# Performance work log

Measured on AMD Instinct MI355X. Metric: run time of the kernel, lower is better.

The kernel has to match this reference:

```python
import jax, jax.numpy as jnp
import numpy as np

B, S, DIN, DOUT = 4, 2048, 4096, 4096

def setup_inputs() -> dict:
    key = jax.random.key(0)
    k1, k2, k3, k4 = jax.random.split(key, 4)
    x = jax.random.normal(k1, (B, S, DIN), dtype=jnp.float32)
    # int8-valued quantized weights in [-127, 127]
    weight_int8 = jax.random.randint(k2, (DOUT, DIN), -127, 128, dtype=jnp.int32).astype(jnp.int8)
    # per-output-row scales, positive, clamped at 1e-8 like the torch code
    weight_scale = jnp.maximum(jax.random.uniform(k3, (DOUT, 1), dtype=jnp.float32) * 0.01, 1e-8)
    bias = jax.random.normal(k4, (DOUT,), dtype=jnp.float32)
    return {"x": x, "weight_int8": weight_int8, "weight_scale": weight_scale, "bias": bias}

def reference(x, weight_int8, weight_scale, bias):
    # Dequantize: [DOUT, DIN] = int8 * per-row scale (broadcast over in_features)
    w = weight_int8.astype(x.dtype) * weight_scale.astype(x.dtype)
    # F.linear: y = x @ w.T + bias
    return jnp.einsum('bsd,od->bso', x, w) + bias
```

## Files before the change

### kernel.cpp

```cpp
#include <hip/hip_runtime.h>
#include <stdint.h>

#define MM 8192
#define NN 4096
#define KK 4096
#define BM 256
#define BN 256
#define BK 64
#define NT (KK / BK)
#define NHALF (4 * NT)

typedef short bf16x8 __attribute__((ext_vector_type(8)));
typedef float f32x4 __attribute__((ext_vector_type(4)));

__device__ __forceinline__ unsigned int f2bf(float f) {
    unsigned int u = __builtin_bit_cast(unsigned int, f);
    u += 0x7FFFu + ((u >> 16) & 1u);
    return u >> 16;
}

__global__ __launch_bounds__(256) void cvt_x_kernel(const float* __restrict__ x,
                                                    unsigned short* __restrict__ xb) {
    int i = blockIdx.x * blockDim.x + threadIdx.x;
    const float4* p = (const float4*)x + (size_t)i * 2;
    float4 a = p[0], b = p[1];
    uint4 o;
    o.x = f2bf(a.x) | (f2bf(a.y) << 16);
    o.y = f2bf(a.z) | (f2bf(a.w) << 16);
    o.z = f2bf(b.x) | (f2bf(b.y) << 16);
    o.w = f2bf(b.z) | (f2bf(b.w) << 16);
    ((uint4*)xb)[i] = o;
}

__global__ __launch_bounds__(256) void cvt_w_kernel(const int* __restrict__ w,
                                                    unsigned short* __restrict__ wb) {
    int i = blockIdx.x * blockDim.x + threadIdx.x;
    const int4* p = (const int4*)w + (size_t)i * 2;
    int4 a = p[0], b = p[1];
    uint4 o;
    o.x = f2bf((float)a.x) | (f2bf((float)a.y) << 16);
    o.y = f2bf((float)a.z) | (f2bf((float)a.w) << 16);
    o.z = f2bf((float)b.x) | (f2bf((float)b.y) << 16);
    o.w = f2bf((float)b.z) | (f2bf((float)b.w) << 16);
    ((uint4*)wb)[i] = o;
}

#define SWZ(q) ((q) ^ ((((q) >> 8) & 7) << 4))

__global__ __launch_bounds__(512, 2) void gemm_kernel(const unsigned short* __restrict__ A,
                                                      const unsigned short* __restrict__ Bt,
                                                      const float* __restrict__ scale,
                                                      const float* __restrict__ bias,
                                                      float* __restrict__ C) {
    __shared__ __align__(16) unsigned short As[2][BM * BK];
    __shared__ __align__(16) unsigned short Bs[2][BN * BK];

    const int nbn = NN / BN;
    const int cpx = ((MM / BM) * (NN / BN)) >> 3;
    int bid = blockIdx.x;
    int swzb = (bid & 7) * cpx + (bid >> 3);
    const int bm = swzb / nbn;
    const int bn = swzb % nbn;

    const int tid  = threadIdx.x;
    const int lane = tid & 63;
    const int wid  = tid >> 6;
    const int wm   = wid >> 2;
    const int wn   = wid & 3;
    const int r    = lane & 15;
    const int kg   = lane >> 4;

    const size_t rowA0 = (size_t)bm * BM;
    const size_t rowB0 = (size_t)bn * BN;

    f32x4 acc[8][4] = {};
    bf16x8 a[4][2], b0[2][2], b1[2][2];

#define STAGE(hid_) do {                                                          \
    int hh = (hid_);                                                              \
    if (hh < NHALF) {                                                             \
        int tt = hh >> 2, h4 = hh & 3;                                            \
        int isA = (h4 == 0) || (h4 == 3);                                         \
        int hi  = (h4 >= 2) ? 1 : 0;                                              \
        int bo  = (tt & 1) * (BM * BK * 2);                                       \
        const unsigned short* gb = isA ? A : Bt;                                  \
        size_t row0 = isA ? rowA0 : rowB0;                                        \
        char* lbase = (isA ? (char*)As : (char*)Bs) + bo + (hi << 14);            \
        _Pragma("unroll")                                                         \
        for (int ii = 0; ii < 2; ++ii) {                                          \
            int q  = (hi << 14) + (ii * 512 + tid) * 16;                          \
            int qs = SWZ(q);                                                      \
            int rw = qs >> 7, cb = qs & 127;                                      \
            const unsigned short* gs = gb + (row0 + rw) * KK + tt * BK + (cb >> 1); \
            char* ld = lbase + (ii * 512 + (wid << 6)) * 16;                      \
            __builtin_amdgcn_global_load_lds(                                     \
                (const __attribute__((address_space(1))) unsigned int*)gs,        \
                (__attribute__((address_space(3))) unsigned int*)ld, 16, 0, 0);   \
        }                                                                         \
    }                                                                             \
} while (0)

#define READ_A(mh_) do {                                                          \
    _Pragma("unroll")                                                             \
    for (int i_ = 0; i_ < 4; ++i_)                                                \
        _Pragma("unroll")                                                         \
        for (int s_ = 0; s_ < 2; ++s_) {                                          \
            int rw = (mh_) * 128 + wm * 64 + i_ * 16 + r;                         \
            int q  = rw * 128 + s_ * 64 + kg * 16;                                \
            a[i_][s_] = *(const bf16x8*)((char*)As + bufo + SWZ(q));              \
        }                                                                         \
} while (0)

#define READ_B(nh_, dst_) do {                                                    \
    _Pragma("unroll")                                                             \
    for (int j_ = 0; j_ < 2; ++j_)                                                \
        _Pragma("unroll")                                                         \
        for (int s_ = 0; s_ < 2; ++s_) {                                          \
            int rw = (nh_) * 128 + wn * 32 + j_ * 16 + r;                         \
            int q  = rw * 128 + s_ * 64 + kg * 16;                                \
            dst_[j_][s_] = *(const bf16x8*)((char*)Bs + bufo + SWZ(q));           \
        }                                                                         \
} while (0)

#define MFMA_Q(mh_, nh_, B_) do {                                                 \
    _Pragma("unroll")                                                             \
    for (int i_ = 0; i_ < 4; ++i_)                                                \
        _Pragma("unroll")                                                         \
        for (int j_ = 0; j_ < 2; ++j_)                                            \
            _Pragma("unroll")                                                     \
            for (int s_ = 0; s_ < 2; ++s_)                                        \
                acc[(mh_) * 4 + i_][(nh_) * 2 + j_] =                             \
                    __builtin_amdgcn_mfma_f32_16x16x32_bf16(                      \
                        a[i_][s_], B_[j_][s_], acc[(mh_) * 4 + i_][(nh_) * 2 + j_], 0, 0, 0); \
} while (0)

    STAGE(0); STAGE(1); STAGE(2); STAGE(3);
    asm volatile("s_waitcnt vmcnt(4)");
    STAGE(4); STAGE(5); STAGE(6);
    asm volatile("s_waitcnt vmcnt(6)");
    __builtin_amdgcn_s_barrier();

    for (int t = 0; t < NT; ++t) {
        const int bufo = (t & 1) * (BM * BK * 2);

        READ_A(0);
        READ_B(0, b0);
        STAGE(4 * t + 7);
        asm volatile("s_waitcnt lgkmcnt(8)");
        __builtin_amdgcn_s_barrier();
        asm volatile("s_waitcnt lgkmcnt(0)");
        __builtin_amdgcn_s_setprio(1);
        MFMA_Q(0, 0, b0);
        __builtin_amdgcn_s_setprio(0);
        __builtin_amdgcn_s_barrier();

        READ_B(1, b1);
        STAGE(4 * t + 8);
        __builtin_amdgcn_s_barrier();
        asm volatile("s_waitcnt lgkmcnt(0)");
        __builtin_amdgcn_s_setprio(1);
        MFMA_Q(0, 1, b1);
        __builtin_amdgcn_s_setprio(0);
        __builtin_amdgcn_s_barrier();

        READ_A(1);
        STAGE(4 * t + 9);
        __builtin_amdgcn_s_barrier();
        asm volatile("s_waitcnt lgkmcnt(0)");
        __builtin_amdgcn_s_setprio(1);
        MFMA_Q(1, 1, b1);
        __builtin_amdgcn_s_setprio(0);
        __builtin_amdgcn_s_barrier();

        STAGE(4 * t + 10);
        __builtin_amdgcn_s_barrier();
        __builtin_amdgcn_s_setprio(1);
        MFMA_Q(1, 0, b0);
        __builtin_amdgcn_s_setprio(0);
        if (t < NT - 1) {
            if (t == NT - 2) asm volatile("s_waitcnt vmcnt(0)");
            else             asm volatile("s_waitcnt vmcnt(6)");
            __builtin_amdgcn_s_barrier();
        }
    }

    const int rj = lane >> 4;
#pragma unroll
    for (int nj = 0; nj < 4; ++nj) {
        int col  = bn * BN + (nj >> 1) * 128 + wn * 32 + (nj & 1) * 16 + r;
        float sc = scale[col];
        float bi = bias[col];
#pragma unroll
        for (int mi = 0; mi < 8; ++mi) {
            int row = bm * BM + (mi >> 2) * 128 + wm * 64 + (mi & 3) * 16 + rj * 4;
#pragma unroll
            for (int j = 0; j < 4; ++j) {
                C[(size_t)(row + j) * NN + col] = acc[mi][nj][j] * sc + bi;
            }
        }
    }
#undef STAGE
#undef READ_A
#undef READ_B
#undef MFMA_Q
}

extern "C" void kernel_launch(void* const* d_in, const int* in_sizes, int n_in,
                              void* d_out, int out_size, void* d_ws, size_t ws_size,
                              hipStream_t stream) {
    const float* x     = (const float*)d_in[0];
    const int*   w8    = (const int*)d_in[1];
    const float* scale = (const float*)d_in[2];
    const float* bias  = (const float*)d_in[3];
    float* out = (float*)d_out;

    unsigned short* xb = (unsigned short*)d_ws;
    unsigned short* wb = xb + (size_t)MM * KK;

    cvt_x_kernel<<<(MM * KK) / 2048, 256, 0, stream>>>(x, xb);
    cvt_w_kernel<<<(NN * KK) / 2048, 256, 0, stream>>>(w8, wb);
    gemm_kernel<<<(MM / BM) * (NN / BN), 512, 0, stream>>>(xb, wb, scale, bias, out);
}
```

Baseline: 540.9 us.

## Fuse conversion kernels and precompute GEMM staging and LDS read addresses

Merges the two fp32/int conversion kernels into one grid-stride kernel, removing one launch. The int32 weight path now reads one int4 per element group. In the GEMM, the per-stage global and LDS address math is precomputed into per-thread offset tables. The main loop is unrolled by two so buffer offsets become compile-time constants, and the MFMA loop order is changed to iterate the k-slice outermost. The aim is to cut scalar/VALU address overhead and loop bookkeeping, at the cost of more registers and a conversion kernel with a fixed grid size.

```diff
diff --git a/kernel.cpp b/kernel.cpp
--- a/kernel.cpp
+++ b/kernel.cpp
@@ -8,7 +8,6 @@
 #define BN 256
 #define BK 64
 #define NT (KK / BK)
-#define NHALF (4 * NT)
 
 typedef short bf16x8 __attribute__((ext_vector_type(8)));
 typedef float f32x4 __attribute__((ext_vector_type(4)));
@@ -19,30 +18,28 @@
     return u >> 16;
 }
 
-__global__ __launch_bounds__(256) void cvt_x_kernel(const float* __restrict__ x,
-                                                    unsigned short* __restrict__ xb) {
-    int i = blockIdx.x * blockDim.x + threadIdx.x;
-    const float4* p = (const float4*)x + (size_t)i * 2;
-    float4 a = p[0], b = p[1];
-    uint4 o;
-    o.x = f2bf(a.x) | (f2bf(a.y) << 16);
-    o.y = f2bf(a.z) | (f2bf(a.w) << 16);
-    o.z = f2bf(b.x) | (f2bf(b.y) << 16);
-    o.w = f2bf(b.z) | (f2bf(b.w) << 16);
-    ((uint4*)xb)[i] = o;
-}
-
-__global__ __launch_bounds__(256) void cvt_w_kernel(const int* __restrict__ w,
-                                                    unsigned short* __restrict__ wb) {
-    int i = blockIdx.x * blockDim.x + threadIdx.x;
-    const int4* p = (const int4*)w + (size_t)i * 2;
-    int4 a = p[0], b = p[1];
-    uint4 o;
-    o.x = f2bf((float)a.x) | (f2bf((float)a.y) << 16);
-    o.y = f2bf((float)a.z) | (f2bf((float)a.w) << 16);
-    o.z = f2bf((float)b.x) | (f2bf((float)b.y) << 16);
-    o.w = f2bf((float)b.z) | (f2bf((float)b.w) << 16);
-    ((uint4*)wb)[i] = o;
+__global__ __launch_bounds__(256) void cvt_kernel(const float* __restrict__ x,
+                                                  const int* __restrict__ w,
+                                                  unsigned short* __restrict__ xb,
+                                                  unsigned short* __restrict__ wb) {
+    const int stride = gridDim.x * blockDim.x;
+    const int tid0 = blockIdx.x * blockDim.x + threadIdx.x;
+    const int nx = MM * KK / 4;
+    for (int i = tid0; i < nx; i += stride) {
+        float4 v = ((const float4*)x)[i];
+        uint2 o;
+        o.x = f2bf(v.x) | (f2bf(v.y) << 16);
+        o.y = f2bf(v.z) | (f2bf(v.w) << 16);
+        ((uint2*)xb)[i] = o;
+    }
+    const int nw = NN * KK / 4;
+    for (int i = tid0; i < nw; i += stride) {
+        int4 v = ((const int4*)w)[i];
+        uint2 o;
+        o.x = f2bf((float)v.x) | (f2bf((float)v.y) << 16);
+        o.y = f2bf((float)v.z) | (f2bf((float)v.w) << 16);
+        ((uint2*)wb)[i] = o;
+    }
 }
 
 #define SWZ(q) ((q) ^ ((((q) >> 8) & 7) << 4))
@@ -70,29 +67,39 @@
     const int r    = lane & 15;
     const int kg   = lane >> 4;
 
-    const size_t rowA0 = (size_t)bm * BM;
-    const size_t rowB0 = (size_t)bn * BN;
+    const int rowA0 = bm * BM;
+    const int rowB0 = bn * BN;
+
+    const int rt0   = (r * 128 + kg * 16) ^ ((r >> 1) << 4);
+    const int offA0 = wm * 8192 + rt0;
+    const int offA1 = offA0 ^ 64;
+    const int offB0 = wn * 4096 + rt0;
+    const int offB1 = offB0 ^ 64;
+    char* Ab = (char*)As;
+    char* Bb = (char*)Bs;
+
+    int goA[2][2], goB[2][2], lo[2][2];
+#pragma unroll
+    for (int hi = 0; hi < 2; ++hi)
+#pragma unroll
+        for (int ii = 0; ii < 2; ++ii) {
+            int q  = (hi << 14) + (ii * 512 + tid) * 16;
+            int qs = SWZ(q);
+            int rw = qs >> 7, cb = qs & 127;
+            goA[hi][ii] = (rowA0 + rw) * (KK * 2) + cb;
+            goB[hi][ii] = (rowB0 + rw) * (KK * 2) + cb;
+            lo[hi][ii]  = (hi << 14) + ii * 8192 + wid * 1024;
+        }
 
     f32x4 acc[8][4] = {};
     bf16x8 a[4][2], b0[2][2], b1[2][2];
 
-#define STAGE(hid_) do {                                                          \
-    int hh = (hid_);                                                              \
-    if (hh < NHALF) {                                                             \
-        int tt = hh >> 2, h4 = hh & 3;                                            \
-        int isA = (h4 == 0) || (h4 == 3);                                         \
-        int hi  = (h4 >= 2) ? 1 : 0;                                              \
-        int bo  = (tt & 1) * (BM * BK * 2);                                       \
-        const unsigned short* gb = isA ? A : Bt;                                  \
-        size_t row0 = isA ? rowA0 : rowB0;                                        \
-        char* lbase = (isA ? (char*)As : (char*)Bs) + bo + (hi << 14);            \
+#define STAGE_A(hi_, tt_, BUFO_) do {                                             \
+    if ((tt_) < NT) {                                                             \
         _Pragma("unroll")                                                         \
         for (int ii = 0; ii < 2; ++ii) {                                          \
-            int q  = (hi << 14) + (ii * 512 + tid) * 16;                          \
-            int qs = SWZ(q);                                                      \
-            int rw = qs >> 7, cb = qs & 127;                                      \
-            const unsigned short* gs = gb + (row0 + rw) * KK + tt * BK + (cb >> 1); \
-            char* ld = lbase + (ii * 512 + (wid << 6)) * 16;                      \
+            const char* gs = (const char*)A + goA[hi_][ii] + (tt_) * 128;         \
+            char* ld = Ab + (BUFO_) + lo[hi_][ii];                                \
             __builtin_amdgcn_global_load_lds(                                     \
                 (const __attribute__((address_space(1))) unsigned int*)gs,        \
                 (__attribute__((address_space(3))) unsigned int*)ld, 16, 0, 0);   \
@@ -100,88 +107,92 @@
     }                                                                             \
 } while (0)
 
-#define READ_A(mh_) do {                                                          \
+#define STAGE_B(hi_, tt_, BUFO_) do {                                             \
+    if ((tt_) < NT) {                                                             \
+        _Pragma("unroll")                                                         \
+        for (int ii = 0; ii < 2; ++ii) {                                          \
+            const char* gs = (const char*)Bt + goB[hi_][ii] + (tt_) * 128;        \
+            char* ld = Bb + (BUFO_) + lo[hi_][ii];                                \
+            __builtin_amdgcn_global_load_lds(                                     \
+                (const __attribute__((address_space(1))) unsigned int*)gs,        \
+                (__attribute__((address_space(3))) unsigned int*)ld, 16, 0, 0);   \
+        }                                                                         \
+    }                                                                             \
+} while (0)
+
+#define READ_A(mh_, BUFO_) do {                                                   \
     _Pragma("unroll")                                                             \
-    for (int i_ = 0; i_ < 4; ++i_)                                                \
-        _Pragma("unroll")                                                         \
-        for (int s_ = 0; s_ < 2; ++s_) {                                          \
-            int rw = (mh_) * 128 + wm * 64 + i_ * 16 + r;                         \
-            int q  = rw * 128 + s_ * 64 + kg * 16;                                \
-            a[i_][s_] = *(const bf16x8*)((char*)As + bufo + SWZ(q));              \
-        }                                                                         \
-} while (0)
-
-#define READ_B(nh_, dst_) do {                                                    \
+    for (int i_ = 0; i_ < 4; ++i_) {                                              \
+        a[i_][0] = *(const bf16x8*)(Ab + (BUFO_) + (mh_) * 16384 + i_ * 2048 + offA0); \
+        a[i_][1] = *(const bf16x8*)(Ab + (BUFO_) + (mh_) * 16384 + i_ * 2048 + offA1); \
+    }                                                                             \
+} while (0)
+
+#define READ_B(nh_, dst_, BUFO_) do {                                             \
     _Pragma("unroll")                                                             \
-    for (int j_ = 0; j_ < 2; ++j_)                                                \
-        _Pragma("unroll")                                                         \
-        for (int s_ = 0; s_ < 2; ++s_) {                                          \
-            int rw = (nh_) * 128 + wn * 32 + j_ * 16 + r;                         \
-            int q  = rw * 128 + s_ * 64 + kg * 16;                                \
-            dst_[j_][s_] = *(const bf16x8*)((char*)Bs + bufo + SWZ(q));           \
-        }                                                                         \
+    for (int j_ = 0; j_ < 2; ++j_) {                                              \
+        dst_[j_][0] = *(const bf16x8*)(Bb + (BUFO_) + (nh_) * 16384 + j_ * 2048 + offB0); \
+        dst_[j_][1] = *(const bf16x8*)(Bb + (BUFO_) + (nh_) * 16384 + j_ * 2048 + offB1); \
+    }                                                                             \
 } while (0)
 
 #define MFMA_Q(mh_, nh_, B_) do {                                                 \
     _Pragma("unroll")                                                             \
-    for (int i_ = 0; i_ < 4; ++i_)                                                \
+    for (int s_ = 0; s_ < 2; ++s_)                                                \
         _Pragma("unroll")                                                         \
-        for (int j_ = 0; j_ < 2; ++j_)                                            \
+        for (int i_ = 0; i_ < 4; ++i_)                                            \
             _Pragma("unroll")                                                     \
-            for (int s_ = 0; s_ < 2; ++s_)                                        \
+            for (int j_ = 0; j_ < 2; ++j_)                                        \
                 acc[(mh_) * 4 + i_][(nh_) * 2 + j_] =                             \
                     __builtin_amdgcn_mfma_f32_16x16x32_bf16(                      \
                         a[i_][s_], B_[j_][s_], acc[(mh_) * 4 + i_][(nh_) * 2 + j_], 0, 0, 0); \
 } while (0)
 
-    STAGE(0); STAGE(1); STAGE(2); STAGE(3);
+#define KTILE(t_, BUFO_, OTHER_) do {                                             \
+    READ_A(0, BUFO_);                                                             \
+    READ_B(0, b0, BUFO_);                                                         \
+    STAGE_A(1, (t_) + 1, OTHER_);                                                 \
+    asm volatile("s_waitcnt lgkmcnt(8)");                                         \
+    __builtin_amdgcn_s_barrier();                                                 \
+    asm volatile("s_waitcnt lgkmcnt(0)");                                         \
+    __builtin_amdgcn_s_setprio(1); MFMA_Q(0, 0, b0); __builtin_amdgcn_s_setprio(0); \
+    __builtin_amdgcn_s_barrier();                                                 \
+    READ_B(1, b1, BUFO_);                                                         \
+    STAGE_A(0, (t_) + 2, BUFO_);                                                  \
+    __builtin_amdgcn_s_barrier();                                                 \
+    asm volatile("s_waitcnt lgkmcnt(0)");                                         \
+    __builtin_amdgcn_s_setprio(1); MFMA_Q(0, 1, b1); __builtin_amdgcn_s_setprio(0); \
+    __builtin_amdgcn_s_barrier();                                                 \
+    READ_A(1, BUFO_);                                                             \
+    STAGE_B(0, (t_) + 2, BUFO_);                                                  \
+    __builtin_amdgcn_s_barrier();                                                 \
+    asm volatile("s_waitcnt lgkmcnt(0)");                                         \
+    __builtin_amdgcn_s_setprio(1); MFMA_Q(1, 1, b1); __builtin_amdgcn_s_setprio(0); \
+    __builtin_amdgcn_s_barrier();                                                 \
+    STAGE_B(1, (t_) + 2, BUFO_);                                                  \
+    __builtin_amdgcn_s_barrier();                                                 \
+    __builtin_amdgcn_s_setprio(1); MFMA_Q(1, 0, b0); __builtin_amdgcn_s_setprio(0); \
+    if ((t_) < NT - 1) {                                                          \
+        if ((t_) == NT - 2) asm volatile("s_waitcnt vmcnt(0)");                   \
+        else                asm volatile("s_waitcnt vmcnt(6)");                   \
+        __builtin_amdgcn_s_barrier();                                             \
+    }                                                                             \
+} while (0)
+
+    STAGE_A(0, 0, 0);
+    STAGE_B(0, 0, 0);
+    STAGE_B(1, 0, 0);
+    STAGE_A(1, 0, 0);
     asm volatile("s_waitcnt vmcnt(4)");
-    STAGE(4); STAGE(5); STAGE(6);
+    STAGE_A(0, 1, 0x8000);
+    STAGE_B(0, 1, 0x8000);
+    STAGE_B(1, 1, 0x8000);
     asm volatile("s_waitcnt vmcnt(6)");
     __builtin_amdgcn_s_barrier();
 
-    for (int t = 0; t < NT; ++t) {
-        const int bufo = (t & 1) * (BM * BK * 2);
-
-        READ_A(0);
-        READ_B(0, b0);
-        STAGE(4 * t + 7);
-        asm volatile("s_waitcnt lgkmcnt(8)");
-        __builtin_amdgcn_s_barrier();
-        asm volatile("s_waitcnt lgkmcnt(0)");
-        __builtin_amdgcn_s_setprio(1);
-        MFMA_Q(0, 0, b0);
-        __builtin_amdgcn_s_setprio(0);
-        __builtin_amdgcn_s_barrier();
-
-        READ_B(1, b1);
-        STAGE(4 * t + 8);
-        __builtin_amdgcn_s_barrier();
-        asm volatile("s_waitcnt lgkmcnt(0)");
-        __builtin_amdgcn_s_setprio(1);
-        MFMA_Q(0, 1, b1);
-        __builtin_amdgcn_s_setprio(0);
-        __builtin_amdgcn_s_barrier();
-
-        READ_A(1);
-        STAGE(4 * t + 9);
-        __builtin_amdgcn_s_barrier();
-        asm volatile("s_waitcnt lgkmcnt(0)");
-        __builtin_amdgcn_s_setprio(1);
-        MFMA_Q(1, 1, b1);
-        __builtin_amdgcn_s_setprio(0);
-        __builtin_amdgcn_s_barrier();
-
-        STAGE(4 * t + 10);
-        __builtin_amdgcn_s_barrier();
-        __builtin_amdgcn_s_setprio(1);
-        MFMA_Q(1, 0, b0);
-        __builtin_amdgcn_s_setprio(0);
-        if (t < NT - 1) {
-            if (t == NT - 2) asm volatile("s_waitcnt vmcnt(0)");
-            else             asm volatile("s_waitcnt vmcnt(6)");
-            __builtin_amdgcn_s_barrier();
-        }
+    for (int t2 = 0; t2 < NT; t2 += 2) {
+        KTILE(t2,     0,      0x8000);
+        KTILE(t2 + 1, 0x8000, 0);
     }
 
     const int rj = lane >> 4;
@@ -199,10 +210,12 @@
             }
         }
     }
-#undef STAGE
+#undef STAGE_A
+#undef STAGE_B
 #undef READ_A
 #undef READ_B
 #undef MFMA_Q
+#undef KTILE
 }
 
 extern "C" void kernel_launch(void* const* d_in, const int* in_sizes, int n_in,
@@ -217,7 +230,6 @@
     unsigned short* xb = (unsigned short*)d_ws;
     unsigned short* wb = xb + (size_t)MM * KK;
 
-    cvt_x_kernel<<<(MM * KK) / 2048, 256, 0, stream>>>(x, xb);
-    cvt_w_kernel<<<(NN * KK) / 2048, 256, 0, stream>>>(w8, wb);
+    cvt_kernel<<<8192, 256, 0, stream>>>(x, w8, xb, wb);
     gemm_kernel<<<(MM / BM) * (NN / BN), 512, 0, stream>>>(xb, wb, scale, bias, out);
 }
```

Measured after the change: 525.0 us. 2.9% less time.
